# Performance work log

Measured on AMD Instinct MI355X. Metric: run time of the kernel, lower is better.

Reference implementation:

```python
import jax, jax.numpy as jnp
import numpy as np

H = 1024
N_HEAD = 16
HEAD = H // N_HEAD
EPS = 1e-12


def setup_inputs() -> dict:
    key = jax.random.key(0)
    ks = jax.random.split(key, 12)
    B, S = 2, 2048
    scale = 1.0 / np.sqrt(H)
    inp = {
        "pre_out": jax.random.normal(ks[0], (B, S, H), dtype=jnp.float32),
        "att_mask": jnp.ones((B, 1, 1, S), dtype=jnp.float32),
        "Wq": jax.random.normal(ks[1], (H, H), dtype=jnp.float32) * scale,
        "bq": jnp.zeros((H,), dtype=jnp.float32),
        "Wk": jax.random.normal(ks[2], (H, H), dtype=jnp.float32) * scale,
        "bk": jnp.zeros((H,), dtype=jnp.float32),
        "Wv": jax.random.normal(ks[3], (H, H), dtype=jnp.float32) * scale,
        "bv": jnp.zeros((H,), dtype=jnp.float32),
        "Wo": jax.random.normal(ks[4], (H, H), dtype=jnp.float32) * scale,
        "bo": jnp.zeros((H,), dtype=jnp.float32),
        "ln_w": jnp.ones((H,), dtype=jnp.float32),
        "ln_b": jnp.zeros((H,), dtype=jnp.float32),
    }
    return inp


def _heads(x):
    # [B,S,H] -> [B,n_head,S,head]
    B, S, _ = x.shape
    return x.reshape(B, S, N_HEAD, HEAD).transpose(0, 2, 1, 3)


def _layernorm(x, w, b):
    u = jnp.mean(x, axis=-1, keepdims=True)
    s = jnp.mean((x - u) ** 2, axis=-1, keepdims=True)
    return w * ((x - u) / jnp.sqrt(s + EPS)) + b


def reference(pre_out, att_mask, Wq, bq, Wk, bk, Wv, bv, Wo, bo, ln_w, ln_b):
    B, S, _ = pre_out.shape
    # torch Linear: y = x @ W.T + b
    Q = _heads(pre_out @ Wq.T + bq)
    K = _heads(pre_out @ Wk.T + bk)
    V = _heads(pre_out @ Wv.T + bv)
    scores = jnp.einsum('bhqd,bhkd->bhqk', Q, K) / np.sqrt(HEAD)
    scores = scores + (1.0 - att_mask) * -10000.0
    prob = jax.nn.softmax(scores, axis=-1)  # eval mode: no dropout
    att = jnp.einsum('bhqk,bhkd->bhqd', prob, V)
    att = att.transpose(0, 2, 1, 3).reshape(B, S, H)
    out = att @ Wo.T + bo
    return _layernorm(pre_out + out, ln_w, ln_b)
```

## Files before the change

kernel.cpp:

```cpp
#include <hip/hip_runtime.h>
#include <math.h>

typedef unsigned short u16;
typedef float floatx4 __attribute__((ext_vector_type(4)));
typedef __bf16 bf16x8 __attribute__((ext_vector_type(8)));
typedef u16 u16x4 __attribute__((ext_vector_type(4)));

#define BB 2
#define SS 2048
#define HH 1024
#define NHEAD 16

__device__ __forceinline__ u16 f2bf(float f) {
  union { float f; unsigned u; } a; a.f = f;
  unsigned r = a.u + 0x7fffu + ((a.u >> 16) & 1u);
  return (u16)(r >> 16);
}

__device__ __forceinline__ u16 bfbits(float f) {
  union { __bf16 h; u16 u; } c; c.h = (__bf16)f; return c.u;
}

__device__ __forceinline__ void gload16(const u16* g, u16* l) {
  __builtin_amdgcn_global_load_lds((const __attribute__((address_space(1))) void*)g,
                                   (__attribute__((address_space(3))) void*)l, 16, 0, 0);
}

__device__ __forceinline__ void fencebar() {
  asm volatile("" ::: "memory");
  __builtin_amdgcn_s_barrier();
  asm volatile("" ::: "memory");
}

__global__ __launch_bounds__(256) void cvt_all(
    const float* __restrict__ X, const float* __restrict__ Wq, const float* __restrict__ Wk,
    const float* __restrict__ Wv, const float* __restrict__ Wo, const float* __restrict__ mask,
    u16* __restrict__ Xb, u16* __restrict__ Wqb, u16* __restrict__ Wkb,
    u16* __restrict__ Wvb, u16* __restrict__ Wob, float* __restrict__ B2) {
  int i = blockIdx.x * 256 + threadIdx.x;
  if (i >= (2 << 20)) {
    int off = i - (2 << 20);
    float4 m = ((const float4*)mask)[off];
    float4 o;
    o.x = (1.0f - m.x) * (-10000.0f * 1.44269504f);
    o.y = (1.0f - m.y) * (-10000.0f * 1.44269504f);
    o.z = (1.0f - m.z) * (-10000.0f * 1.44269504f);
    o.w = (1.0f - m.w) * (-10000.0f * 1.44269504f);
    ((float4*)B2)[off] = o;
    return;
  }
  const float* src; u16* dst; int off;
  if (i < (1 << 20)) { src = X; dst = Xb; off = i; }
  else {
    int j = i - (1 << 20);
    int m = j >> 18; off = j & ((1 << 18) - 1);
    src = (m == 0) ? Wq : (m == 1) ? Wk : (m == 2) ? Wv : Wo;
    dst = (m == 0) ? Wqb : (m == 1) ? Wkb : (m == 2) ? Wvb : Wob;
  }
  float4 v = ((const float4*)src)[off];
  u16x4 p; p.x = f2bf(v.x); p.y = f2bf(v.y); p.z = f2bf(v.z); p.w = f2bf(v.w);
  ((u16x4*)dst)[off] = p;
}

__global__ __launch_bounds__(256) void qkv_gemm(
    const u16* __restrict__ X,
    const u16* __restrict__ Wq, const u16* __restrict__ Wk, const u16* __restrict__ Wv,
    const float* __restrict__ bq, const float* __restrict__ bk, const float* __restrict__ bv,
    u16* __restrict__ Qo, u16* __restrict__ Ko, u16* __restrict__ Vt) {
  __shared__ u16 As[2][128 * 32];
  __shared__ u16 Ws[2][128 * 32];

  const int tid = threadIdx.x;
  const int w = tid >> 6, lane = tid & 63, quad = lane >> 4, l15 = lane & 15;
  const int L = blockIdx.y * 24 + blockIdx.x;
  const int wid = (L & 7) * 96 + (L >> 3);
  const int bx = wid % 24, by = wid / 24;
  const int mat = bx >> 3;
  const int col0 = (bx & 7) * 128;
  const int row0 = by * 128;
  const u16* W = (mat == 0) ? Wq : (mat == 1) ? Wk : Wv;
  const float* bias = (mat == 0) ? bq : (mat == 1) ? bk : bv;

  const int c0 = tid, c1 = tid + 256;
  const int ar0 = c0 >> 2, al0 = ((c0 & 3) ^ (ar0 & 3)) * 8;
  const int ar1 = c1 >> 2, al1 = ((c1 & 3) ^ (ar1 & 3)) * 8;
  const u16* gA0 = X + (row0 + ar0) * HH + al0;
  const u16* gA1 = X + (row0 + ar1) * HH + al1;
  const u16* gW0 = W + (col0 + ar0) * HH + al0;
  const u16* gW1 = W + (col0 + ar1) * HH + al1;

  const int wm = (w >> 1) * 64, wn = (w & 1) * 64;
  const int sw = quad ^ (l15 & 3);
  const int aoff = (wm + l15) * 32 + sw * 8;
  const int boff = (wn + l15) * 32 + sw * 8;

  auto stage = [&](int buf, int k0) {
    gload16(gA0 + k0, As[buf] + c0 * 8);
    gload16(gA1 + k0, As[buf] + c1 * 8);
    gload16(gW0 + k0, Ws[buf] + c0 * 8);
    gload16(gW1 + k0, Ws[buf] + c1 * 8);
  };

  floatx4 acc[4][4];
#pragma unroll
  for (int i = 0; i < 4; i++)
#pragma unroll
    for (int j = 0; j < 4; j++) acc[i][j] = {0.f, 0.f, 0.f, 0.f};

  stage(0, 0);

  for (int kt = 0; kt < 32; kt++) {
    const int cur = kt & 1;
    if (kt < 31) {
      stage(cur ^ 1, (kt + 1) * 32);
      asm volatile("s_waitcnt vmcnt(4)" ::: "memory");
    } else {
      asm volatile("s_waitcnt vmcnt(0)" ::: "memory");
    }
    fencebar();

    bf16x8 af[4], bfr[4];
#pragma unroll
    for (int i = 0; i < 4; i++) af[i] = *(const bf16x8*)(As[cur] + aoff + i * 512);
#pragma unroll
    for (int j = 0; j < 4; j++) bfr[j] = *(const bf16x8*)(Ws[cur] + boff + j * 512);
    __builtin_amdgcn_s_setprio(1);
#pragma unroll
    for (int i = 0; i < 4; i++)
#pragma unroll
      for (int j = 0; j < 4; j++)
        acc[i][j] = __builtin_amdgcn_mfma_f32_16x16x32_bf16(af[i], bfr[j], acc[i][j], 0, 0, 0);
    __builtin_amdgcn_s_setprio(0);

    fencebar();
  }

  const int rb = row0 + wm + quad * 4;
  if (mat < 2) {
    u16* O = (mat == 0) ? Qo : Ko;
#pragma unroll
    for (int j = 0; j < 4; j++) {
      const int col = col0 + wn + j * 16 + l15;
      const float bj = bias[col];
#pragma unroll
      for (int i = 0; i < 4; i++) {
        const int r0 = rb + i * 16;
#pragma unroll
        for (int r = 0; r < 4; r++)
          O[(r0 + r) * HH + col] = bfbits(acc[i][j][r] + bj);
      }
    }
  } else {
#pragma unroll
    for (int j = 0; j < 4; j++) {
      const int col = col0 + wn + j * 16 + l15;
      const float bj = bias[col];
      const int h = col >> 6, d = col & 63;
#pragma unroll
      for (int i = 0; i < 4; i++) {
        const int m0 = rb + i * 16;
        const int b = m0 >> 11, s = m0 & 2047;
        u16x4 pk;
#pragma unroll
        for (int r = 0; r < 4; r++) pk[r] = bfbits(acc[i][j][r] + bj);
        *(u16x4*)(Vt + (((b * NHEAD + h) * 64 + d) * SS + s)) = pk;
      }
    }
  }
}

__global__ __launch_bounds__(256) void oproj_gemm(
    const u16* __restrict__ A, const u16* __restrict__ W,
    const float* __restrict__ bias, float* __restrict__ Y) {
  __shared__ u16 As[2][128 * 32];
  __shared__ u16 Ws[2][64 * 32];

  const int tid = threadIdx.x;
  const int w = tid >> 6, lane = tid & 63, quad = lane >> 4, l15 = lane & 15;
  const int L = blockIdx.y * 16 + blockIdx.x;
  const int wid = (L & 7) * 64 + (L >> 3);
  const int col0 = (wid & 15) * 64;
  const int row0 = (wid >> 4) * 128;

  const int c0 = tid, c1 = tid + 256;
  const int ar0 = c0 >> 2, al0 = ((c0 & 3) ^ (ar0 & 3)) * 8;
  const int ar1 = c1 >> 2, al1 = ((c1 & 3) ^ (ar1 & 3)) * 8;
  const u16* gA0 = A + (row0 + ar0) * HH + al0;
  const u16* gA1 = A + (row0 + ar1) * HH + al1;
  const u16* gW0 = W + (col0 + ar0) * HH + al0;

  const int wm = w * 32;
  const int sw = quad ^ (l15 & 3);
  const int aoff = (wm + l15) * 32 + sw * 8;
  const int boff = l15 * 32 + sw * 8;

  auto stage = [&](int buf, int k0) {
    gload16(gA0 + k0, As[buf] + c0 * 8);
    gload16(gA1 + k0, As[buf] + c1 * 8);
    gload16(gW0 + k0, Ws[buf] + c0 * 8);
  };

  floatx4 acc[2][4];
#pragma unroll
  for (int i = 0; i < 2; i++)
#pragma unroll
    for (int j = 0; j < 4; j++) acc[i][j] = {0.f, 0.f, 0.f, 0.f};

  stage(0, 0);

  for (int kt = 0; kt < 32; kt++) {
    const int cur = kt & 1;
    if (kt < 31) {
      stage(cur ^ 1, (kt + 1) * 32);
      asm volatile("s_waitcnt vmcnt(3)" ::: "memory");
    } else {
      asm volatile("s_waitcnt vmcnt(0)" ::: "memory");
    }
    fencebar();

    bf16x8 af[2], bfr[4];
#pragma unroll
    for (int i = 0; i < 2; i++) af[i] = *(const bf16x8*)(As[cur] + aoff + i * 512);
#pragma unroll
    for (int j = 0; j < 4; j++) bfr[j] = *(const bf16x8*)(Ws[cur] + boff + j * 512);
    __builtin_amdgcn_s_setprio(1);
#pragma unroll
    for (int i = 0; i < 2; i++)
#pragma unroll
      for (int j = 0; j < 4; j++)
        acc[i][j] = __builtin_amdgcn_mfma_f32_16x16x32_bf16(af[i], bfr[j], acc[i][j], 0, 0, 0);
    __builtin_amdgcn_s_setprio(0);

    fencebar();
  }

  const int rb = row0 + wm + quad * 4;
#pragma unroll
  for (int j = 0; j < 4; j++) {
    const int col = col0 + j * 16 + l15;
    const float bj = bias[col];
#pragma unroll
    for (int i = 0; i < 2; i++) {
      const int r0 = rb + i * 16;
#pragma unroll
      for (int r = 0; r < 4; r++)
        Y[(r0 + r) * HH + col] = acc[i][j][r] + bj;
    }
  }
}

#define QT 128

__global__ __launch_bounds__(512, 4) void attn_mfma(
    const u16* __restrict__ Q, const u16* __restrict__ K, const u16* __restrict__ Vt,
    const float* __restrict__ B2, u16* __restrict__ O) {
  __shared__ u16 SMEM[34816];
  u16* const UQ = SMEM;
  u16* const KB = SMEM + 10240;
  u16* const VB = SMEM + 22528;

  const int L = blockIdx.y * 16 + blockIdx.x;
  const int wid = (L & 7) * 64 + (L >> 3);
  const int qt = wid & 15, bh = wid >> 4;
  const int b = bh >> 4, h = bh & 15;
  const int tid = threadIdx.x;
  const int w = tid >> 6, lane = tid & 63, quad = lane >> 4, l15 = lane & 15;
  const int sw = l15 & 7;
  const int qg = w & 3;
  const int khalf = w >> 2;
  const int koff = khalf * 32;
  const int kh4 = khalf * 4;

  const int qbase  = (b * SS + qt * QT) * HH + h * 64;
  const int kvbase = (b * SS) * HH + h * 64;
  const int vtbase = (b * NHEAD + h) * 64 * SS;

  auto stage_kv = [&](int bi, int t) {
    const int c = tid;
    const int r = c >> 3, lc = (c & 7) ^ (r & 7);
    gload16(K + kvbase + (t * 64 + r) * HH + lc * 8, KB + bi * 4096 + c * 8);
    gload16(Vt + vtbase + r * SS + t * 64 + lc * 8, VB + bi * 4096 + c * 8);
  };

#pragma unroll
  for (int i = 0; i < 2; i++) {
    const int c = tid + i * 512;
    const int r = c >> 3, lc = (c & 7) ^ (r & 7);
    gload16(Q + qbase + r * HH + lc * 8, UQ + c * 8);
  }
  stage_kv(0, 0);
  stage_kv(1, 1);
  asm volatile("s_waitcnt vmcnt(4)" ::: "memory");
  fencebar();

  bf16x8 aQ[2][2];
#pragma unroll
  for (int mt = 0; mt < 2; mt++) {
    const u16* qr = UQ + (qg * 32 + mt * 16 + l15) * 64;
    aQ[mt][0] = *(const bf16x8*)(qr + ((quad ^ sw) * 8));
    aQ[mt][1] = *(const bf16x8*)(qr + (((4 + quad) ^ sw) * 8));
  }
  asm volatile("s_waitcnt lgkmcnt(0)" ::: "memory");

  floatx4 o[2][4];
#pragma unroll
  for (int mt = 0; mt < 2; mt++)
#pragma unroll
    for (int j = 0; j < 4; j++) o[mt][j] = {0.f, 0.f, 0.f, 0.f};
  float lp[2] = {0.f, 0.f};

  u16* const Pw = UQ + w * 1280;
  const float* B2row = B2 + b * SS;

  for (int kt = 0; kt < 32; kt++) {
    const int cI = kt % 3;

    fencebar();

    const float* B2k = B2row + kt * 64 + koff;
    floatx4 bb[2];
    bb[0] = *(const floatx4*)(B2k + quad * 4);
    bb[1] = *(const floatx4*)(B2k + 16 + quad * 4);
    asm volatile("" ::: "memory");

    if (kt < 30) {
      stage_kv((kt + 2) % 3, kt + 2);
      asm volatile("s_waitcnt vmcnt(2)" ::: "memory");
    } else {
      asm volatile("s_waitcnt vmcnt(0)" ::: "memory");
    }

    const u16* Kc = KB + cI * 4096;
    const u16* Vc = VB + cI * 4096;

    floatx4 st[2][2];
    __builtin_amdgcn_s_setprio(1);
#pragma unroll
    for (int kb = 0; kb < 2; kb++) {
      const u16* kr = Kc + (koff + kb * 16 + l15) * 64;
      bf16x8 kf0 = *(const bf16x8*)(kr + ((quad ^ sw) * 8));
      bf16x8 kf1 = *(const bf16x8*)(kr + (((4 + quad) ^ sw) * 8));
#pragma unroll
      for (int mt = 0; mt < 2; mt++) {
        floatx4 z = {0.f, 0.f, 0.f, 0.f};
        z = __builtin_amdgcn_mfma_f32_16x16x32_bf16(kf0, aQ[mt][0], z, 0, 0, 0);
        st[mt][kb] = __builtin_amdgcn_mfma_f32_16x16x32_bf16(kf1, aQ[mt][1], z, 0, 0, 0);
      }
    }
    __builtin_amdgcn_s_setprio(0);

#pragma unroll
    for (int kb = 0; kb < 2; kb++) {
#pragma unroll
      for (int mt = 0; mt < 2; mt++) {
        u16x4 pk;
#pragma unroll
        for (int r = 0; r < 4; r++) {
          const float p = __builtin_amdgcn_exp2f(st[mt][kb][r] * 0.180336880f + bb[kb][r]);
          lp[mt] += p;
          pk[r] = bfbits(p);
        }
        *(u16x4*)(Pw + (mt * 16 + l15) * 40 + kb * 16 + quad * 4) = pk;
      }
    }

    bf16x8 pa[2];
#pragma unroll
    for (int mt = 0; mt < 2; mt++)
      pa[mt] = *(const bf16x8*)(Pw + (mt * 16 + l15) * 40 + quad * 8);
    __builtin_amdgcn_s_setprio(1);
#pragma unroll
    for (int j = 0; j < 4; j++) {
      const u16* vr = Vc + (j * 16 + l15) * 64;
      bf16x8 vf = *(const bf16x8*)(vr + (((kh4 + quad) ^ sw) * 8));
#pragma unroll
      for (int mt = 0; mt < 2; mt++)
        o[mt][j] = __builtin_amdgcn_mfma_f32_16x16x32_bf16(pa[mt], vf, o[mt][j], 0, 0, 0);
    }
    __builtin_amdgcn_s_setprio(0);
  }

  fencebar();

#pragma unroll
  for (int mt = 0; mt < 2; mt++) {
    float v = lp[mt];
    v += __shfl_xor(v, 16);
    v += __shfl_xor(v, 32);
    lp[mt] = v;
  }

  float* const oS  = (float*)(SMEM + 10240);
  float* const lpS = (float*)SMEM;
  if (w >= 4) {
    float* pb = oS + (w - 4) * 2048;
#pragma unroll
    for (int mt = 0; mt < 2; mt++) {
#pragma unroll
      for (int j = 0; j < 4; j++)
#pragma unroll
        for (int r = 0; r < 4; r++)
          pb[(mt * 16 + quad * 4 + r) * 64 + j * 16 + l15] = o[mt][j][r];
      if (quad == 0) lpS[qg * 32 + mt * 16 + l15] = lp[mt];
    }
  }
  asm volatile("s_waitcnt lgkmcnt(0)" ::: "memory");
  fencebar();

  if (w < 4) {
    const float* pb = oS + w * 2048;
    float lpt[2];
#pragma unroll
    for (int mt = 0; mt < 2; mt++)
      lpt[mt] = lp[mt] + lpS[w * 32 + mt * 16 + l15];
#pragma unroll
    for (int mt = 0; mt < 2; mt++) {
      const int orow0 = b * SS + qt * QT + qg * 32 + mt * 16 + quad * 4;
#pragma unroll
      for (int r = 0; r < 4; r++) {
        const float inv = 1.0f / __shfl(lpt[mt], quad * 4 + r);
#pragma unroll
        for (int j = 0; j < 4; j++) {
          const float val = o[mt][j][r] + pb[(mt * 16 + quad * 4 + r) * 64 + j * 16 + l15];
          O[(orow0 + r) * HH + h * 64 + j * 16 + l15] = bfbits(val * inv);
        }
      }
    }
  }
}

__global__ __launch_bounds__(256) void add_layernorm(
    const float* __restrict__ x0, const float* __restrict__ y,
    const float* __restrict__ w, const float* __restrict__ b,
    float* __restrict__ out) {
  const int row = blockIdx.x * 4 + (threadIdx.x >> 6);
  const int l = threadIdx.x & 63;
  const float4* xr = (const float4*)(x0 + (size_t)row * HH);
  const float4* yr = (const float4*)(y + (size_t)row * HH);

  float4 v[4];
  float s = 0.f;
#pragma unroll
  for (int i = 0; i < 4; i++) {
    const float4 a = xr[l + i * 64];
    const float4 c = yr[l + i * 64];
    v[i].x = a.x + c.x; v[i].y = a.y + c.y;
    v[i].z = a.z + c.z; v[i].w = a.w + c.w;
    s += v[i].x + v[i].y + v[i].z + v[i].w;
  }
#pragma unroll
  for (int o = 1; o < 64; o <<= 1) s += __shfl_xor(s, o);
  const float mean = s * (1.0f / HH);

  float sq = 0.f;
#pragma unroll
  for (int i = 0; i < 4; i++) {
    const float dx = v[i].x - mean, dy = v[i].y - mean;
    const float dz = v[i].z - mean, dw = v[i].w - mean;
    sq += dx * dx + dy * dy + dz * dz + dw * dw;
  }
#pragma unroll
  for (int o = 1; o < 64; o <<= 1) sq += __shfl_xor(sq, o);
  const float inv = rsqrtf(sq * (1.0f / HH) + 1e-12f);

  float4* orow = (float4*)(out + (size_t)row * HH);
#pragma unroll
  for (int i = 0; i < 4; i++) {
    const float4 ww = ((const float4*)w)[l + i * 64];
    const float4 bb = ((const float4*)b)[l + i * 64];
    float4 o4;
    o4.x = ww.x * ((v[i].x - mean) * inv) + bb.x;
    o4.y = ww.y * ((v[i].y - mean) * inv) + bb.y;
    o4.z = ww.z * ((v[i].z - mean) * inv) + bb.z;
    o4.w = ww.w * ((v[i].w - mean) * inv) + bb.w;
    orow[l + i * 64] = o4;
  }
}

extern "C" void kernel_launch(void* const* d_in, const int* in_sizes, int n_in,
                              void* d_out, int out_size, void* d_ws, size_t ws_size,
                              hipStream_t stream) {
  const float* pre_out = (const float*)d_in[0];
  const float* mask    = (const float*)d_in[1];
  const float* Wq = (const float*)d_in[2];
  const float* bq = (const float*)d_in[3];
  const float* Wk = (const float*)d_in[4];
  const float* bk = (const float*)d_in[5];
  const float* Wv = (const float*)d_in[6];
  const float* bv = (const float*)d_in[7];
  const float* Wo = (const float*)d_in[8];
  const float* bo = (const float*)d_in[9];
  const float* ln_w = (const float*)d_in[10];
  const float* ln_b = (const float*)d_in[11];
  float* out = (float*)d_out;

  u16* Xb  = (u16*)d_ws;
  u16* Wqb = Xb + (4 << 20);
  u16* Wkb = Wqb + (1 << 20);
  u16* Wvb = Wkb + (1 << 20);
  u16* Wob = Wvb + (1 << 20);
  u16* Qb  = Wob + (1 << 20);
  u16* Kb  = Qb + (4 << 20);
  u16* Vtb = Kb + (4 << 20);
  u16* Ab  = Vtb + (4 << 20);
  float* Yb = (float*)(Ab + (4 << 20));
  float* B2 = Yb + (4 << 20);

  cvt_all<<<8196, 256, 0, stream>>>(pre_out, Wq, Wk, Wv, Wo, mask,
                                    Xb, Wqb, Wkb, Wvb, Wob, B2);

  qkv_gemm<<<dim3(24, 32), 256, 0, stream>>>(Xb, Wqb, Wkb, Wvb, bq, bk, bv, Qb, Kb, Vtb);

  attn_mfma<<<dim3(SS / QT, BB * NHEAD), 512, 0, stream>>>(Qb, Kb, Vtb, B2, Ab);

  oproj_gemm<<<dim3(16, 32), 256, 0, stream>>>(Ab, Wob, bo, Yb);

  add_layernorm<<<BB * SS / 4, 256, 0, stream>>>(pre_out, Yb, ln_w, ln_b, out);
}
```

Baseline: 206.6 us.

## Keep softmax probabilities in registers and permute V fragment loads to match

```diff
diff --git a/kernel.cpp b/kernel.cpp
--- a/kernel.cpp
+++ b/kernel.cpp
@@ -19,6 +19,12 @@
 
 __device__ __forceinline__ u16 bfbits(float f) {
   union { __bf16 h; u16 u; } c; c.h = (__bf16)f; return c.u;
+}
+
+__device__ __forceinline__ unsigned cvtpk(float lo, float hi) {
+  unsigned r;
+  asm("v_cvt_pk_bf16_f32 %0, %1, %2" : "=v"(r) : "v"(lo), "v"(hi));
+  return r;
 }
 
 __device__ __forceinline__ void gload16(const u16* g, u16* l) {
@@ -254,10 +260,10 @@
 __global__ __launch_bounds__(512, 4) void attn_mfma(
     const u16* __restrict__ Q, const u16* __restrict__ K, const u16* __restrict__ Vt,
     const float* __restrict__ B2, u16* __restrict__ O) {
-  __shared__ u16 SMEM[34816];
+  __shared__ u16 SMEM[32768];
   u16* const UQ = SMEM;
-  u16* const KB = SMEM + 10240;
-  u16* const VB = SMEM + 22528;
+  u16* const KB = SMEM + 8192;
+  u16* const VB = SMEM + 20480;
 
   const int L = blockIdx.y * 16 + blockIdx.x;
   const int wid = (L & 7) * 64 + (L >> 3);
@@ -269,7 +275,6 @@
   const int qg = w & 3;
   const int khalf = w >> 2;
   const int koff = khalf * 32;
-  const int kh4 = khalf * 4;
 
   const int qbase  = (b * SS + qt * QT) * HH + h * 64;
   const int kvbase = (b * SS) * HH + h * 64;
@@ -300,7 +305,6 @@
     aQ[mt][0] = *(const bf16x8*)(qr + ((quad ^ sw) * 8));
     aQ[mt][1] = *(const bf16x8*)(qr + (((4 + quad) ^ sw) * 8));
   }
-  asm volatile("s_waitcnt lgkmcnt(0)" ::: "memory");
 
   floatx4 o[2][4];
 #pragma unroll
@@ -309,8 +313,10 @@
     for (int j = 0; j < 4; j++) o[mt][j] = {0.f, 0.f, 0.f, 0.f};
   float lp[2] = {0.f, 0.f};
 
-  u16* const Pw = UQ + w * 1280;
   const float* B2row = B2 + b * SS;
+
+  const int vc0 = khalf * 4 + (quad >> 1);
+  const int vsub = (quad & 1) * 4;
 
   for (int kt = 0; kt < 32; kt++) {
     const int cI = kt % 3;
@@ -349,33 +355,35 @@
     }
     __builtin_amdgcn_s_setprio(0);
 
-#pragma unroll
-    for (int kb = 0; kb < 2; kb++) {
-#pragma unroll
-      for (int mt = 0; mt < 2; mt++) {
-        u16x4 pk;
+    bf16x8 pa[2];
+#pragma unroll
+    for (int mt = 0; mt < 2; mt++) {
+      float pe[2][4];
+#pragma unroll
+      for (int kb = 0; kb < 2; kb++)
 #pragma unroll
         for (int r = 0; r < 4; r++) {
-          const float p = __builtin_amdgcn_exp2f(st[mt][kb][r] * 0.180336880f + bb[kb][r]);
-          lp[mt] += p;
-          pk[r] = bfbits(p);
+          pe[kb][r] = __builtin_amdgcn_exp2f(st[mt][kb][r] * 0.180336880f + bb[kb][r]);
+          lp[mt] += pe[kb][r];
         }
-        *(u16x4*)(Pw + (mt * 16 + l15) * 40 + kb * 16 + quad * 4) = pk;
-      }
-    }
-
-    bf16x8 pa[2];
-#pragma unroll
-    for (int mt = 0; mt < 2; mt++)
-      pa[mt] = *(const bf16x8*)(Pw + (mt * 16 + l15) * 40 + quad * 8);
+      union { unsigned wd[4]; bf16x8 v; } pu;
+      pu.wd[0] = cvtpk(pe[0][0], pe[0][1]);
+      pu.wd[1] = cvtpk(pe[0][2], pe[0][3]);
+      pu.wd[2] = cvtpk(pe[1][0], pe[1][1]);
+      pu.wd[3] = cvtpk(pe[1][2], pe[1][3]);
+      pa[mt] = pu.v;
+    }
+
     __builtin_amdgcn_s_setprio(1);
 #pragma unroll
     for (int j = 0; j < 4; j++) {
-      const u16* vr = Vc + (j * 16 + l15) * 64;
-      bf16x8 vf = *(const bf16x8*)(vr + (((kh4 + quad) ^ sw) * 8));
+      const u16* vrow = Vc + (j * 16 + l15) * 64 + vsub;
+      union { u16x4 hh[2]; bf16x8 v; } vu;
+      vu.hh[0] = *(const u16x4*)(vrow + ((vc0 ^ sw) * 8));
+      vu.hh[1] = *(const u16x4*)(vrow + (((vc0 + 2) ^ sw) * 8));
 #pragma unroll
       for (int mt = 0; mt < 2; mt++)
-        o[mt][j] = __builtin_amdgcn_mfma_f32_16x16x32_bf16(pa[mt], vf, o[mt][j], 0, 0, 0);
+        o[mt][j] = __builtin_amdgcn_mfma_f32_16x16x32_bf16(pa[mt], vu.v, o[mt][j], 0, 0, 0);
     }
     __builtin_amdgcn_s_setprio(0);
   }
@@ -390,7 +398,7 @@
     lp[mt] = v;
   }
 
-  float* const oS  = (float*)(SMEM + 10240);
+  float* const oS  = (float*)(SMEM + 8192);
   float* const lpS = (float*)SMEM;
   if (w >= 4) {
     float* pb = oS + (w - 4) * 2048;
```

After: 207.9 us. Within noise of the previous version (+0.6%).
